# Performance work log

Measured on AMD Instinct MI355X. Metric: run time of the kernel, lower is better.

## Reference

```python
import jax, jax.numpy as jnp
import numpy as np

D = 512
H = 8
DH = D // H
FF = 2048
E = 4
EPS = 1e-5


def _layernorm(x, g, b):
    mu = jnp.mean(x, axis=-1, keepdims=True)
    var = jnp.mean(jnp.square(x - mu), axis=-1, keepdims=True)
    return (x - mu) * jax.lax.rsqrt(var + EPS) * g + b


def setup_inputs() -> dict:
    key = jax.random.key(0)
    ks = jax.random.split(key, 12)
    B, T = 4, 2048
    s = 0.02
    return {
        "x": jax.random.normal(ks[0], (B, T, D), jnp.float32),
        "fourier_bias": jax.random.normal(ks[1], (B, T, T), jnp.float32) * 0.1,
        "Wk": jax.random.normal(ks[2], (D, D), jnp.float32) * s,
        "bk": jnp.zeros((D,), jnp.float32),
        "Wv": jax.random.normal(ks[3], (D, D), jnp.float32) * s,
        "bv": jnp.zeros((D,), jnp.float32),
        "Wo": jax.random.normal(ks[4], (D, D), jnp.float32) * s,
        "bo": jnp.zeros((D,), jnp.float32),
        "ln1_g": jnp.ones((D,), jnp.float32),
        "ln1_b": jnp.zeros((D,), jnp.float32),
        "Wg": jax.random.normal(ks[5], (D, E), jnp.float32) * s,
        "bg": jnp.zeros((E,), jnp.float32),
        "W1": jax.random.normal(ks[6], (E, D, FF), jnp.float32) * s,
        "b1": jnp.zeros((E, FF), jnp.float32),
        "W2": jax.random.normal(ks[7], (E, FF, D), jnp.float32) * s,
        "b2": jnp.zeros((E, D), jnp.float32),
        "ln2_g": jnp.ones((D,), jnp.float32),
        "ln2_b": jnp.zeros((D,), jnp.float32),
    }


def reference(x, fourier_bias, Wk, bk, Wv, bv, Wo, bo, ln1_g, ln1_b,
              Wg, bg, W1, b1, W2, b2, ln2_g, ln2_b):
    B, T, _ = x.shape
    # --- Fourier pairwise-bias "attention" ---
    K = (x @ Wk + bk).reshape(B, T, H, DH).transpose(0, 2, 1, 3)  # [B,H,T,Dh]
    V = (x @ Wv + bv).reshape(B, T, H, DH).transpose(0, 2, 1, 3)  # [B,H,T,Dh]
    # sum_j (K_j + fb_ij) * V_j = sum_j K_j*V_j  +  sum_j fb_ij * V_j
    kv_sum = jnp.sum(K * V, axis=2, keepdims=True)                # [B,H,1,Dh]
    fbV = jnp.einsum('bij,bhjd->bhid', fourier_bias, V)           # [B,H,T,Dh]
    wv = (kv_sum + fbV).transpose(0, 2, 1, 3).reshape(B, T, D)
    x = _layernorm(x + (wv @ Wo + bo), ln1_g, ln1_b)
    # --- MoE FFN, top-2 gating (dropout/noise inactive in eval) ---
    scores = jax.nn.softmax(x @ Wg + bg, axis=-1)                 # [B,T,E]
    vals, idx = jax.lax.top_k(scores, 2)                          # [B,T,2]
    w = (jax.nn.one_hot(idx[..., 0], E, dtype=x.dtype) * vals[..., 0:1]
         + jax.nn.one_hot(idx[..., 1], E, dtype=x.dtype) * vals[..., 1:2])  # [B,T,E]
    h = jax.nn.relu(jnp.einsum('btd,edf->btef', x, W1) + b1)      # [B,T,E,FF]
    y = jnp.einsum('btef,efd->bted', h, W2) + b2                  # [B,T,E,D]
    ff = jnp.einsum('bte,bted->btd', w, y)
    return _layernorm(x + ff, ln2_g, ln2_b)
```

## Files before the change

kernel.cpp:

```cpp
#include <hip/hip_runtime.h>
#include <stdint.h>

#define BB   4
#define TT   2048
#define DD   512
#define FFF  2048
#define NEXP 4
#define NTOK (BB*TT)
#define LNEPS 1e-5f

typedef unsigned short u16;
typedef __attribute__((ext_vector_type(8))) short bf16x8;
typedef __attribute__((ext_vector_type(4))) float f32x4;

__device__ __forceinline__ u16 f2bf(float f) {
  union { float f; unsigned u; } v; v.f = f;
  return (u16)((v.u + 0x7FFFu + ((v.u >> 16) & 1u)) >> 16);
}
__device__ __forceinline__ float bf2f(u16 h) {
  union { unsigned u; float f; } v; v.u = (unsigned)h << 16; return v.f;
}

__device__ __forceinline__ void gl2lds(const u16* g, u16* l) {
  __builtin_amdgcn_global_load_lds(
      (const __attribute__((address_space(1))) void*)g,
      (__attribute__((address_space(3))) void*)l, 16, 0, 0);
}


__global__ void split_f32_kernel(const float* __restrict__ in, u16* __restrict__ hi,
                                 u16* __restrict__ lo, int n4) {
  int i = blockIdx.x * blockDim.x + threadIdx.x;
  if (i >= n4) return;
  float4 f = ((const float4*)in)[i];
  u16 h0 = f2bf(f.x), h1 = f2bf(f.y), h2 = f2bf(f.z), h3 = f2bf(f.w);
  u16 l0 = f2bf(f.x - bf2f(h0)), l1 = f2bf(f.y - bf2f(h1));
  u16 l2 = f2bf(f.z - bf2f(h2)), l3 = f2bf(f.w - bf2f(h3));
  ((uint2*)hi)[i] = uint2{(unsigned)h0 | ((unsigned)h1 << 16), (unsigned)h2 | ((unsigned)h3 << 16)};
  ((uint2*)lo)[i] = uint2{(unsigned)l0 | ((unsigned)l1 << 16), (unsigned)l2 | ((unsigned)l3 << 16)};
}

__global__ void transpose_split3_kernel(const float* __restrict__ s0, const float* __restrict__ s1,
                                        const float* __restrict__ s2,
                                        u16* __restrict__ kvhi, u16* __restrict__ kvlo,
                                        u16* __restrict__ ohi,  u16* __restrict__ olo) {
  __shared__ float tile[32][33];
  const int z = blockIdx.z;
  const float* in = (z == 0) ? s0 : (z == 1) ? s1 : s2;
  int c0 = blockIdx.x * 32, r0 = blockIdx.y * 32;
  int tx = threadIdx.x, ty = threadIdx.y;
#pragma unroll
  for (int k = 0; k < 4; k++)
    tile[ty + 8*k][tx] = in[(size_t)(r0 + ty + 8*k) * DD + c0 + tx];
  __syncthreads();
#pragma unroll
  for (int k = 0; k < 4; k++) {
    float v = tile[tx][ty + 8*k];
    u16 h = f2bf(v);
    u16 l = f2bf(v - bf2f(h));
    const int c = c0 + ty + 8*k;
    if (z < 2) {
      size_t idx = (size_t)(2*c + z) * DD + r0 + tx;
      kvhi[idx] = h; kvlo[idx] = l;
    } else {
      size_t idx = (size_t)c * DD + r0 + tx;
      ohi[idx] = h; olo[idx] = l;
    }
  }
}

__global__ void transpose_cast_kernel(const float* __restrict__ in, u16* __restrict__ out,
                                      int R, int C) {
  __shared__ float tile[32][33];
  int z = blockIdx.z;
  in  += (size_t)z * R * C;
  out += (size_t)z * R * C;
  int c0 = blockIdx.x * 32, r0 = blockIdx.y * 32;
  int tx = threadIdx.x, ty = threadIdx.y;
#pragma unroll
  for (int k = 0; k < 4; k++)
    tile[ty + 8*k][tx] = in[(size_t)(r0 + ty + 8*k) * C + c0 + tx];
  __syncthreads();
#pragma unroll
  for (int k = 0; k < 4; k++)
    out[(size_t)(c0 + ty + 8*k) * R + r0 + tx] = f2bf(tile[tx][ty + 8*k]);
}

template<int MODE>
__global__ __launch_bounds__(256)
void gemm_split2_kernel(const u16* __restrict__ Ahi, const u16* __restrict__ Alo,
                        const u16* __restrict__ Bhi, const u16* __restrict__ Blo,
                        const float* __restrict__ bias0, const float* __restrict__ bias1,
                        float* __restrict__ out0,
                        u16* __restrict__ outh, u16* __restrict__ outl,
                        int M, int N, int K,
                        long long sA, long long sB, long long sO) {
  constexpr int NBUF = (MODE == 2) ? 2 : 1;
  __shared__ u16 AhL[NBUF][128*32], AlL[NBUF][128*32];
  __shared__ u16 BhL[NBUF][64*32],  BlL[NBUF][64*32];

  int mt, nt, z;
  if constexpr (MODE == 2) {
    const int gid = blockIdx.x;
    const int xcd = gid & 7, slot = gid >> 3;
    z  = xcd >> 1;
    mt = (xcd & 1) + 2 * (slot >> 3);
    nt = slot & 7;
  } else {
    mt = blockIdx.x; nt = blockIdx.y; z = blockIdx.z;
  }
  const int m0 = mt * 128, n0 = nt * 64;

  Ahi += (size_t)z * sA; Alo += (size_t)z * sA;
  Bhi += (size_t)z * sB; Blo += (size_t)z * sB;
  const int tid = threadIdx.x;
  const int lane = tid & 63, wave = tid >> 6;
  const int wm = wave >> 1, wn = wave & 1;
  const int quad = lane >> 4, l16 = lane & 15;
  const int sxor = ((l16 >> 1) & 3) << 3;

  const int ar1 = tid >> 2;
  const int ac1 = (((tid & 3) ^ ((tid >> 3) & 3)) << 3);
  const u16* pAh1 = Ahi + (size_t)(m0 + ar1) * K + ac1;
  const u16* pAh2 = Ahi + (size_t)(m0 + ar1 + 64) * K + ac1;
  const u16* pAl1 = Alo + (size_t)(m0 + ar1) * K + ac1;
  const u16* pAl2 = Alo + (size_t)(m0 + ar1 + 64) * K + ac1;
  const u16* pBh1 = Bhi + (size_t)(n0 + ar1) * K + ac1;
  const u16* pBl1 = Blo + (size_t)(n0 + ar1) * K + ac1;
  const int wofs = wave * 512;

  f32x4 acc[4][2];
#pragma unroll
  for (int i = 0; i < 4; i++)
#pragma unroll
    for (int j = 0; j < 2; j++)
      acc[i][j] = f32x4{0.f, 0.f, 0.f, 0.f};

  const int NIT = K >> 5;
  if constexpr (MODE == 2) {
    gl2lds(pAh1, &AhL[0][wofs]); gl2lds(pAh2, &AhL[0][2048 + wofs]);
    gl2lds(pAl1, &AlL[0][wofs]); gl2lds(pAl2, &AlL[0][2048 + wofs]);
    gl2lds(pBh1, &BhL[0][wofs]); gl2lds(pBl1, &BlL[0][wofs]);
    for (int it = 0; it < NIT; it++) {
      const int buf = it & 1;
      __syncthreads();
      if (it + 1 < NIT) {
        const int ko = (it + 1) << 5;
        gl2lds(pAh1 + ko, &AhL[buf ^ 1][wofs]); gl2lds(pAh2 + ko, &AhL[buf ^ 1][2048 + wofs]);
        gl2lds(pAl1 + ko, &AlL[buf ^ 1][wofs]); gl2lds(pAl2 + ko, &AlL[buf ^ 1][2048 + wofs]);
        gl2lds(pBh1 + ko, &BhL[buf ^ 1][wofs]); gl2lds(pBl1 + ko, &BlL[buf ^ 1][wofs]);
      }
      bf16x8 afh[4], afl[4], bqh[2], bql[2];
#pragma unroll
      for (int i = 0; i < 4; i++) {
        afh[i] = *(const bf16x8*)&AhL[buf][(wm*64 + i*16 + l16) * 32 + (quad*8 ^ sxor)];
        afl[i] = *(const bf16x8*)&AlL[buf][(wm*64 + i*16 + l16) * 32 + (quad*8 ^ sxor)];
      }
#pragma unroll
      for (int j = 0; j < 2; j++) {
        bqh[j] = *(const bf16x8*)&BhL[buf][(wn*32 + j*16 + l16) * 32 + (quad*8 ^ sxor)];
        bql[j] = *(const bf16x8*)&BlL[buf][(wn*32 + j*16 + l16) * 32 + (quad*8 ^ sxor)];
      }
#pragma unroll
      for (int i = 0; i < 4; i++)
#pragma unroll
        for (int j = 0; j < 2; j++) {
          acc[i][j] = __builtin_amdgcn_mfma_f32_16x16x32_bf16(afh[i], bqh[j], acc[i][j], 0, 0, 0);
          acc[i][j] = __builtin_amdgcn_mfma_f32_16x16x32_bf16(afh[i], bql[j], acc[i][j], 0, 0, 0);
          acc[i][j] = __builtin_amdgcn_mfma_f32_16x16x32_bf16(afl[i], bqh[j], acc[i][j], 0, 0, 0);
        }
    }
  } else {
    for (int it = 0; it < NIT; it++) {
      const int ko = it << 5;
      __syncthreads();
      gl2lds(pAh1 + ko, &AhL[0][wofs]); gl2lds(pAh2 + ko, &AhL[0][2048 + wofs]);
      gl2lds(pAl1 + ko, &AlL[0][wofs]); gl2lds(pAl2 + ko, &AlL[0][2048 + wofs]);
      gl2lds(pBh1 + ko, &BhL[0][wofs]); gl2lds(pBl1 + ko, &BlL[0][wofs]);
      __syncthreads();
      bf16x8 afh[4], afl[4], bqh[2], bql[2];
#pragma unroll
      for (int i = 0; i < 4; i++) {
        afh[i] = *(const bf16x8*)&AhL[0][(wm*64 + i*16 + l16) * 32 + (quad*8 ^ sxor)];
        afl[i] = *(const bf16x8*)&AlL[0][(wm*64 + i*16 + l16) * 32 + (quad*8 ^ sxor)];
      }
#pragma unroll
      for (int j = 0; j < 2; j++) {
        bqh[j] = *(const bf16x8*)&BhL[0][(wn*32 + j*16 + l16) * 32 + (quad*8 ^ sxor)];
        bql[j] = *(const bf16x8*)&BlL[0][(wn*32 + j*16 + l16) * 32 + (quad*8 ^ sxor)];
      }
#pragma unroll
      for (int i = 0; i < 4; i++)
#pragma unroll
        for (int j = 0; j < 2; j++) {
          acc[i][j] = __builtin_amdgcn_mfma_f32_16x16x32_bf16(afh[i], bqh[j], acc[i][j], 0, 0, 0);
          acc[i][j] = __builtin_amdgcn_mfma_f32_16x16x32_bf16(afh[i], bql[j], acc[i][j], 0, 0, 0);
          acc[i][j] = __builtin_amdgcn_mfma_f32_16x16x32_bf16(afl[i], bqh[j], acc[i][j], 0, 0, 0);
        }
    }
  }

  if constexpr (MODE == 1) {
    const int b = m0 >> 11;
    const int rb0 = m0 & (TT - 1);
    const int colbase = n0 + wn*32 + l16;
    float kvp[2] = {0.f, 0.f};
#pragma unroll
    for (int i = 0; i < 4; i++) {
#pragma unroll
      for (int j = 0; j < 2; j++) {
        const int col = colbase + j*16;
        const int d = col >> 1;
        float vals[4];
#pragma unroll
        for (int r = 0; r < 4; r++) {
          float vv = acc[i][j][r] + ((col & 1) ? bias1[d] : bias0[d]);
          float pa = __shfl_xor(vv, 1);
          if (!(col & 1)) kvp[j] += vv * pa;
          vals[r] = vv;
        }
        if (col & 1) {
          const int rr = rb0 + wm*64 + i*16 + quad*4;
          u16 hs[4], ls[4];
#pragma unroll
          for (int r = 0; r < 4; r++) {
            hs[r] = f2bf(vals[r]);
            ls[r] = f2bf(vals[r] - bf2f(hs[r]));
          }
          size_t o = (size_t)b * DD * TT + (size_t)d * TT + rr;
          *(uint2*)&outh[o] = uint2{(unsigned)hs[0] | ((unsigned)hs[1]<<16),
                                    (unsigned)hs[2] | ((unsigned)hs[3]<<16)};
          *(uint2*)&outl[o] = uint2{(unsigned)ls[0] | ((unsigned)ls[1]<<16),
                                    (unsigned)ls[2] | ((unsigned)ls[3]<<16)};
        }
      }
    }
#pragma unroll
    for (int j = 0; j < 2; j++) {
      float p = kvp[j];
      p += __shfl_xor(p, 16);
      p += __shfl_xor(p, 32);
      const int col = colbase + j*16;
      if (!(col & 1) && quad == 0)
        atomicAdd(&out0[b * DD + (col >> 1)], p);
    }
  } else {
#pragma unroll
    for (int i = 0; i < 4; i++) {
#pragma unroll
      for (int r = 0; r < 4; r++) {
        const int row = m0 + wm*64 + i*16 + quad*4 + r;
#pragma unroll
        for (int j = 0; j < 2; j++) {
          const int col = n0 + wn*32 + j*16 + l16;
          float v = acc[i][j][r];
          if constexpr (MODE == 0) {
            out0[(size_t)row * N + col] = v + bias0[col];
          } else {
            v += bias0[(size_t)z * DD + col];
            u16 hv = f2bf(v);
            size_t idx = (size_t)z * sO + (size_t)row * DD + col;
            outh[idx] = hv;
            outl[idx] = f2bf(v - bf2f(hv));
          }
        }
      }
    }
  }
}

__global__ __launch_bounds__(256)
void moe_gemm1_kernel(const u16* __restrict__ X, const int* __restrict__ tokl,
                      const int* __restrict__ cnt, const u16* __restrict__ W1t,
                      const float* __restrict__ b1, u16* __restrict__ H) {
  const int e = blockIdx.z;
  int base = 0, cnte = 0;
#pragma unroll
  for (int i = 0; i < NEXP; i++) { int c = cnt[i]; if (i < e) base += c; if (i == e) cnte = c; }
  const int m0 = blockIdx.x * 128;
  if (m0 >= cnte) return;
  __shared__ u16 As[2][128*32], Bs[2][128*32];
  const int n0 = blockIdx.y * 128;
  const int tid = threadIdx.x, lane = tid & 63, wave = tid >> 6;
  const int wm = wave >> 1, wn = wave & 1, quad = lane >> 4, l16 = lane & 15;
  const int sxor = ((l16 >> 1) & 3) << 3;
  const int ar1 = tid >> 2;
  const int ac1 = (((tid & 3) ^ ((tid >> 3) & 3)) << 3);
  const int i1 = m0 + ar1 < cnte ? m0 + ar1 : cnte - 1;
  const int i2 = m0 + ar1 + 64 < cnte ? m0 + ar1 + 64 : cnte - 1;
  const int t1 = tokl[e * NTOK + i1], t2 = tokl[e * NTOK + i2];
  const u16* Bt = W1t + (size_t)e * DD * FFF;
  const float* bias = b1 + (size_t)e * FFF;
  const u16* pA1 = X + (size_t)t1 * DD + ac1;
  const u16* pA2 = X + (size_t)t2 * DD + ac1;
  const u16* pB1 = Bt + (size_t)(n0 + ar1) * DD + ac1;
  const u16* pB2 = Bt + (size_t)(n0 + ar1 + 64) * DD + ac1;
  const int wofs = wave * 512;

  f32x4 acc[4][4];
#pragma unroll
  for (int i = 0; i < 4; i++)
#pragma unroll
    for (int j = 0; j < 4; j++)
      acc[i][j] = f32x4{0.f, 0.f, 0.f, 0.f};

  const int NIT = DD >> 5;
  gl2lds(pA1, &As[0][wofs]); gl2lds(pA2, &As[0][2048 + wofs]);
  gl2lds(pB1, &Bs[0][wofs]); gl2lds(pB2, &Bs[0][2048 + wofs]);
  for (int it = 0; it < NIT; it++) {
    const int buf = it & 1;
    __syncthreads();
    if (it + 1 < NIT) {
      const int ko = (it + 1) << 5;
      gl2lds(pA1 + ko, &As[buf ^ 1][wofs]); gl2lds(pA2 + ko, &As[buf ^ 1][2048 + wofs]);
      gl2lds(pB1 + ko, &Bs[buf ^ 1][wofs]); gl2lds(pB2 + ko, &Bs[buf ^ 1][2048 + wofs]);
    }
    bf16x8 af[4], bq[4];
#pragma unroll
    for (int i = 0; i < 4; i++)
      af[i] = *(const bf16x8*)&As[buf][(wm*64 + i*16 + l16)*32 + (quad*8 ^ sxor)];
#pragma unroll
    for (int j = 0; j < 4; j++)
      bq[j] = *(const bf16x8*)&Bs[buf][(wn*64 + j*16 + l16)*32 + (quad*8 ^ sxor)];
#pragma unroll
    for (int i = 0; i < 4; i++)
#pragma unroll
      for (int j = 0; j < 4; j++)
        acc[i][j] = __builtin_amdgcn_mfma_f32_16x16x32_bf16(af[i], bq[j], acc[i][j], 0, 0, 0);
  }

#pragma unroll
  for (int i = 0; i < 4; i++) {
#pragma unroll
    for (int r = 0; r < 4; r++) {
      const int m = m0 + wm*64 + i*16 + quad*4 + r;
      if (m < cnte) {
#pragma unroll
        for (int j = 0; j < 4; j++) {
          const int col = n0 + wn*64 + j*16 + l16;
          H[(size_t)(base + m) * FFF + col] = f2bf(fmaxf(acc[i][j][r] + bias[col], 0.f));
        }
      }
    }
  }
}

__global__ __launch_bounds__(256)
void moe_gemm2_kernel(const u16* __restrict__ H, const int* __restrict__ tokl,
                      const int* __restrict__ cnt, const u16* __restrict__ W2t,
                      const float* __restrict__ b2, const float* __restrict__ wgt,
                      u16* __restrict__ Y) {
  const int e = blockIdx.z;
  int base = 0, cnte = 0;
#pragma unroll
  for (int i = 0; i < NEXP; i++) { int c = cnt[i]; if (i < e) base += c; if (i == e) cnte = c; }
  const int m0 = blockIdx.x * 128;
  if (m0 >= cnte) return;
  __shared__ u16 As[2][128*32], Bs[2][128*32];
  const int n0 = blockIdx.y * 128;
  const int tid = threadIdx.x, lane = tid & 63, wave = tid >> 6;
  const int wm = wave >> 1, wn = wave & 1, quad = lane >> 4, l16 = lane & 15;
  const int sxor = ((l16 >> 1) & 3) << 3;
  const int ar1 = tid >> 2;
  const int ac1 = (((tid & 3) ^ ((tid >> 3) & 3)) << 3);
  const int i1 = m0 + ar1 < cnte ? m0 + ar1 : cnte - 1;
  const int i2 = m0 + ar1 + 64 < cnte ? m0 + ar1 + 64 : cnte - 1;
  const u16* Bt = W2t + (size_t)e * FFF * DD;
  const float* bias = b2 + (size_t)e * DD;
  const u16* pA1 = H + (size_t)(base + i1) * FFF + ac1;
  const u16* pA2 = H + (size_t)(base + i2) * FFF + ac1;
  const u16* pB1 = Bt + (size_t)(n0 + ar1) * FFF + ac1;
  const u16* pB2 = Bt + (size_t)(n0 + ar1 + 64) * FFF + ac1;
  const int wofs = wave * 512;

  f32x4 acc[4][4];
#pragma unroll
  for (int i = 0; i < 4; i++)
#pragma unroll
    for (int j = 0; j < 4; j++)
      acc[i][j] = f32x4{0.f, 0.f, 0.f, 0.f};

  const int NIT = FFF >> 5;
  gl2lds(pA1, &As[0][wofs]); gl2lds(pA2, &As[0][2048 + wofs]);
  gl2lds(pB1, &Bs[0][wofs]); gl2lds(pB2, &Bs[0][2048 + wofs]);
  for (int it = 0; it < NIT; it++) {
    const int buf = it & 1;
    __syncthreads();
    if (it + 1 < NIT) {
      const int ko = (it + 1) << 5;
      gl2lds(pA1 + ko, &As[buf ^ 1][wofs]); gl2lds(pA2 + ko, &As[buf ^ 1][2048 + wofs]);
      gl2lds(pB1 + ko, &Bs[buf ^ 1][wofs]); gl2lds(pB2 + ko, &Bs[buf ^ 1][2048 + wofs]);
    }
    bf16x8 af[4], bq[4];
#pragma unroll
    for (int i = 0; i < 4; i++)
      af[i] = *(const bf16x8*)&As[buf][(wm*64 + i*16 + l16)*32 + (quad*8 ^ sxor)];
#pragma unroll
    for (int j = 0; j < 4; j++)
      bq[j] = *(const bf16x8*)&Bs[buf][(wn*64 + j*16 + l16)*32 + (quad*8 ^ sxor)];
#pragma unroll
    for (int i = 0; i < 4; i++)
#pragma unroll
      for (int j = 0; j < 4; j++)
        acc[i][j] = __builtin_amdgcn_mfma_f32_16x16x32_bf16(af[i], bq[j], acc[i][j], 0, 0, 0);
  }

#pragma unroll
  for (int i = 0; i < 4; i++) {
#pragma unroll
    for (int r = 0; r < 4; r++) {
      const int m = m0 + wm*64 + i*16 + quad*4 + r;
      if (m < cnte) {
        const int t = tokl[e * NTOK + m];
        const float w = wgt[(size_t)t * NEXP + e];
#pragma unroll
        for (int j = 0; j < 4; j++) {
          const int col = n0 + wn*64 + j*16 + l16;
          Y[(size_t)(base + m) * DD + col] = f2bf((acc[i][j][r] + bias[col]) * w);
        }
      }
    }
  }
}

__global__ void ln_kernel(const float* __restrict__ a, const float* __restrict__ b,
                          const float* __restrict__ g, const float* __restrict__ beta,
                          float* __restrict__ outf, u16* __restrict__ outb) {
  int t = blockIdx.x;
  int tid = threadIdx.x;
  float v0 = a[(size_t)t*DD + tid]       + b[(size_t)t*DD + tid];
  float v1 = a[(size_t)t*DD + 256 + tid] + b[(size_t)t*DD + 256 + tid];
  float s = v0 + v1, s2 = v0*v0 + v1*v1;
  for (int off = 32; off; off >>= 1) { s += __shfl_down(s, off); s2 += __shfl_down(s2, off); }
  __shared__ float ws[4], ws2[4];
  if ((tid & 63) == 0) { ws[tid >> 6] = s; ws2[tid >> 6] = s2; }
  __syncthreads();
  if (tid == 0) {
    float ts = 0, ts2 = 0;
    for (int i = 0; i < 4; i++) { ts += ws[i]; ts2 += ws2[i]; }
    ws[0] = ts; ws2[0] = ts2;
  }
  __syncthreads();
  float mean = ws[0] * (1.f / DD);
  float var  = ws2[0] * (1.f / DD) - mean * mean;
  float rstd = rsqrtf(var + LNEPS);
  float o0 = (v0 - mean) * rstd * g[tid]       + beta[tid];
  float o1 = (v1 - mean) * rstd * g[256 + tid] + beta[256 + tid];
  outf[(size_t)t*DD + tid]       = o0;
  outf[(size_t)t*DD + 256 + tid] = o1;
  outb[(size_t)t*DD + tid]       = f2bf(o0);
  outb[(size_t)t*DD + 256 + tid] = f2bf(o1);
}

__global__ void ln2_kernel(const float* __restrict__ x1, const u16* __restrict__ Y,
                           const int* __restrict__ tokslot, const int* __restrict__ cnt,
                           const float* __restrict__ g, const float* __restrict__ beta,
                           float* __restrict__ out) {
  int t = blockIdx.x;
  int tid = threadIdx.x;
  const int c0 = cnt[0], c1 = cnt[1], c2 = cnt[2];
  const int s0 = tokslot[2*t], s1 = tokslot[2*t + 1];
  const int e0 = s0 >> 14, k0 = s0 & 16383;
  const int e1 = s1 >> 14, k1 = s1 & 16383;
  const int b0 = (e0 > 0 ? c0 : 0) + (e0 > 1 ? c1 : 0) + (e0 > 2 ? c2 : 0);
  const int b1 = (e1 > 0 ? c0 : 0) + (e1 > 1 ? c1 : 0) + (e1 > 2 ? c2 : 0);
  const u16* y0 = Y + (size_t)(b0 + k0) * DD;
  const u16* y1 = Y + (size_t)(b1 + k1) * DD;
  float v0 = x1[(size_t)t*DD + tid]       + bf2f(y0[tid])       + bf2f(y1[tid]);
  float v1 = x1[(size_t)t*DD + 256 + tid] + bf2f(y0[256 + tid]) + bf2f(y1[256 + tid]);
  float s = v0 + v1, s2 = v0*v0 + v1*v1;
  for (int off = 32; off; off >>= 1) { s += __shfl_down(s, off); s2 += __shfl_down(s2, off); }
  __shared__ float ws[4], ws2[4];
  if ((tid & 63) == 0) { ws[tid >> 6] = s; ws2[tid >> 6] = s2; }
  __syncthreads();
  if (tid == 0) {
    float ts = 0, ts2 = 0;
    for (int i = 0; i < 4; i++) { ts += ws[i]; ts2 += ws2[i]; }
    ws[0] = ts; ws2[0] = ts2;
  }
  __syncthreads();
  float mean = ws[0] * (1.f / DD);
  float var  = ws2[0] * (1.f / DD) - mean * mean;
  float rstd = rsqrtf(var + LNEPS);
  out[(size_t)t*DD + tid]       = (v0 - mean) * rstd * g[tid]       + beta[tid];
  out[(size_t)t*DD + 256 + tid] = (v1 - mean) * rstd * g[256 + tid] + beta[256 + tid];
}

__global__ __launch_bounds__(256)
void gate_kernel(const float* __restrict__ x1, const float* __restrict__ Wg,
                 const float* __restrict__ bg, float* __restrict__ wfull,
                 int* __restrict__ tokl, int* __restrict__ cnt, int* __restrict__ tokslot) {
  __shared__ int lcnt[NEXP];
  __shared__ int lbase[NEXP];
  __shared__ int lslots[NEXP][128];
  const int tid = threadIdx.x, lane = tid & 63, wave = tid >> 6;
  if (tid < NEXP) lcnt[tid] = 0;
  __syncthreads();
  const int tblk = blockIdx.x * 64;
  for (int i = 0; i < 16; i++) {
    const int t = tblk + wave * 16 + i;
    float s0 = 0.f, s1 = 0.f, s2 = 0.f, s3 = 0.f;
    for (int d = lane; d < DD; d += 64) {
      float xv = x1[(size_t)t * DD + d];
      float4 w = *(const float4*)&Wg[d * 4];
      s0 += xv * w.x; s1 += xv * w.y; s2 += xv * w.z; s3 += xv * w.w;
    }
    for (int off = 32; off; off >>= 1) {
      s0 += __shfl_down(s0, off); s1 += __shfl_down(s1, off);
      s2 += __shfl_down(s2, off); s3 += __shfl_down(s3, off);
    }
    if (lane == 0) {
      float sc[4] = {s0 + bg[0], s1 + bg[1], s2 + bg[2], s3 + bg[3]};
      float mx = fmaxf(fmaxf(sc[0], sc[1]), fmaxf(sc[2], sc[3]));
      float sum = 0.f;
      for (int e = 0; e < 4; e++) { sc[e] = expf(sc[e] - mx); sum += sc[e]; }
      float inv = 1.f / sum;
      for (int e = 0; e < 4; e++) sc[e] *= inv;
      int i0 = 0;
      for (int e = 1; e < 4; e++) if (sc[e] > sc[i0]) i0 = e;
      int i1 = -1;
      for (int e = 0; e < 4; e++) { if (e == i0) continue; if (i1 < 0 || sc[e] > sc[i1]) i1 = e; }
      float w[4] = {0.f, 0.f, 0.f, 0.f};
      w[i0] = sc[i0]; w[i1] = sc[i1];
      *(float4*)&wfull[(size_t)t * 4] = float4{w[0], w[1], w[2], w[3]};
      int p0 = atomicAdd(&lcnt[i0], 1); lslots[i0][p0] = (t << 1);
      int p1 = atomicAdd(&lcnt[i1], 1); lslots[i1][p1] = (t << 1) | 1;
    }
  }
  __syncthreads();
  if (tid < NEXP) lbase[tid] = atomicAdd(&cnt[tid], lcnt[tid]);
  __syncthreads();
  for (int idx = tid; idx < NEXP * 128; idx += 256) {
    const int e = idx >> 7, p = idx & 127;
    if (p < lcnt[e]) {
      const int v = lslots[e][p];
      const int t = v >> 1;
      const int pos = lbase[e] + p;
      tokl[e * NTOK + pos] = t;
      tokslot[2 * t + (v & 1)] = (e << 14) | pos;
    }
  }
}

extern "C" void kernel_launch(void* const* d_in, const int* in_sizes, int n_in,
                              void* d_out, int out_size, void* d_ws, size_t ws_size,
                              hipStream_t stream) {
  const float* x    = (const float*)d_in[0];
  const float* fb   = (const float*)d_in[1];
  const float* Wk   = (const float*)d_in[2];
  const float* bk   = (const float*)d_in[3];
  const float* Wv   = (const float*)d_in[4];
  const float* bv   = (const float*)d_in[5];
  const float* Wo   = (const float*)d_in[6];
  const float* bo   = (const float*)d_in[7];
  const float* ln1g = (const float*)d_in[8];
  const float* ln1b = (const float*)d_in[9];
  const float* Wg   = (const float*)d_in[10];
  const float* bg   = (const float*)d_in[11];
  const float* W1   = (const float*)d_in[12];
  const float* b1   = (const float*)d_in[13];
  const float* W2   = (const float*)d_in[14];
  const float* b2   = (const float*)d_in[15];
  const float* ln2g = (const float*)d_in[16];
  const float* ln2b = (const float*)d_in[17];

  const size_t MiB = 1048576;
  char* ws = (char*)d_ws;
  char* R1 = ws;
  u16* xhi  = (u16*)R1;             u16* xlo  = (u16*)(R1 + 8*MiB);
  u16* wvhi = (u16*)R1;             u16* wvlo = (u16*)(R1 + 8*MiB);
  u16* x1b  = (u16*)R1;
  char* R2 = ws + 16*MiB;
  u16* fbhi = (u16*)R2;             u16* fblo = (u16*)(R2 + 32*MiB);
  u16* h    = (u16*)R2;
  char* R3 = ws + 80*MiB;
  u16* vthi   = (u16*)R3;           u16* vtlo  = (u16*)(R3 + 8*MiB);
  float* attn = (float*)R3;
  u16*  yb    = (u16*)R3;
  float* x1f  = (float*)(R3 + 16*MiB);
  char* R4 = ws + 112*MiB;
  u16* wkvthi = (u16*)R4;
  u16* wkvtlo = (u16*)(R4 + 1*MiB);
  u16* wothi  = (u16*)(R4 + 2*MiB);
  u16* wotlo  = (u16*)(R4 + 2*MiB + 512*1024);
  u16* w1t    = (u16*)(R4 + 3*MiB);
  u16* w2t    = (u16*)(R4 + 11*MiB);
  char* R5 = ws + 131*MiB;
  float* kvs    = (float*)R5;
  int*   cnt    = (int*)(R5 + 8192);
  float* wfull  = (float*)(R5 + 16*1024);
  int*   tokl   = (int*)(R5 + 160*1024);
  int*   tokslot= (int*)(R5 + 320*1024);
  (void)ws_size; (void)in_sizes; (void)n_in; (void)out_size;

  dim3 tb(32, 8);

  hipMemsetAsync(kvs, 0, 8192 + 16, stream);

  split_f32_kernel<<<NTOK * DD / 4 / 256, 256, 0, stream>>>(x, xhi, xlo, NTOK * DD / 4);
  split_f32_kernel<<<BB * TT * TT / 4 / 256, 256, 0, stream>>>(fb, fbhi, fblo, BB * TT * TT / 4);
  transpose_split3_kernel<<<dim3(16, 16, 3), tb, 0, stream>>>(Wk, Wv, Wo,
                                                              wkvthi, wkvtlo, wothi, wotlo);
  transpose_cast_kernel<<<dim3(FFF/32, DD/32, NEXP), tb, 0, stream>>>(W1, w1t, DD, FFF);
  transpose_cast_kernel<<<dim3(DD/32, FFF/32, NEXP), tb, 0, stream>>>(W2, w2t, FFF, DD);

  gemm_split2_kernel<1><<<dim3(64, 16, 1), 256, 0, stream>>>(
      xhi, xlo, wkvthi, wkvtlo, bk, bv, kvs, vthi, vtlo,
      NTOK, 2*DD, DD, 0, 0, 0);

  gemm_split2_kernel<2><<<dim3(512, 1, 1), 256, 0, stream>>>(
      fbhi, fblo, vthi, vtlo, kvs, nullptr, nullptr, wvhi, wvlo,
      TT, DD, TT, (long long)TT*TT, (long long)DD*TT, (long long)TT*DD);

  gemm_split2_kernel<0><<<dim3(64, 8, 1), 256, 0, stream>>>(
      wvhi, wvlo, wothi, wotlo, bo, nullptr, attn, nullptr, nullptr,
      NTOK, DD, DD, 0, 0, 0);

  ln_kernel<<<NTOK, 256, 0, stream>>>(x, attn, ln1g, ln1b, x1f, x1b);

  gate_kernel<<<NTOK / 64, 256, 0, stream>>>(x1f, Wg, bg, wfull, tokl, cnt, tokslot);

  moe_gemm1_kernel<<<dim3(NTOK/128, FFF/128, NEXP), 256, 0, stream>>>(
      x1b, tokl, cnt, w1t, b1, h);
  moe_gemm2_kernel<<<dim3(NTOK/128, DD/128, NEXP), 256, 0, stream>>>(
      h, tokl, cnt, w2t, b2, wfull, yb);

  ln2_kernel<<<NTOK, 256, 0, stream>>>(x1f, yb, tokslot, cnt, ln2g, ln2b, (float*)d_out);
}
```

Measured before the change: 510.7 us.

## Fuse fourier_bias hi/lo split into the fbV GEMM operand load

Removes the separate pass that split the 64 MiB fp32 fourier_bias into bf16 hi/lo arrays. A dedicated fbV kernel now loads fp32 tiles directly into LDS and splits them into hi/lo bf16 fragments in registers, using packed convert instructions. This drops one full read and 32 MiB of writes plus a later 32 MiB re-read of the split arrays. In exchange the A tile in LDS is twice as large, each K step does extra ALU conversion work, and the generic GEMM loses its MODE 2 path.

```diff
diff --git a/kernel.cpp b/kernel.cpp
--- a/kernel.cpp
+++ b/kernel.cpp
@@ -25,6 +25,40 @@
   __builtin_amdgcn_global_load_lds(
       (const __attribute__((address_space(1))) void*)g,
       (__attribute__((address_space(3))) void*)l, 16, 0, 0);
+}
+__device__ __forceinline__ void gl2lds_f(const float* g, float* l) {
+  __builtin_amdgcn_global_load_lds(
+      (const __attribute__((address_space(1))) void*)g,
+      (__attribute__((address_space(3))) void*)l, 16, 0, 0);
+}
+
+__device__ __forceinline__ unsigned cvtpk_bf16(float a, float b) {
+  unsigned r;
+  asm volatile("v_cvt_pk_bf16_f32 %0, %1, %2" : "=v"(r) : "v"(a), "v"(b));
+  return r;
+}
+__device__ __forceinline__ void split2x4(f32x4 a0, f32x4 a1, bf16x8* hi, bf16x8* lo) {
+  union U { unsigned u[4]; bf16x8 v; };
+  U H, L;
+  H.u[0] = cvtpk_bf16(a0[0], a0[1]);
+  H.u[1] = cvtpk_bf16(a0[2], a0[3]);
+  H.u[2] = cvtpk_bf16(a1[0], a1[1]);
+  H.u[3] = cvtpk_bf16(a1[2], a1[3]);
+  union F { unsigned u; float f; } t0, t1;
+  float l0,l1,l2,l3,l4,l5,l6,l7;
+  t0.u = H.u[0] << 16;         l0 = a0[0] - t0.f;
+  t1.u = H.u[0] & 0xffff0000u; l1 = a0[1] - t1.f;
+  t0.u = H.u[1] << 16;         l2 = a0[2] - t0.f;
+  t1.u = H.u[1] & 0xffff0000u; l3 = a0[3] - t1.f;
+  t0.u = H.u[2] << 16;         l4 = a1[0] - t0.f;
+  t1.u = H.u[2] & 0xffff0000u; l5 = a1[1] - t1.f;
+  t0.u = H.u[3] << 16;         l6 = a1[2] - t0.f;
+  t1.u = H.u[3] & 0xffff0000u; l7 = a1[3] - t1.f;
+  L.u[0] = cvtpk_bf16(l0, l1);
+  L.u[1] = cvtpk_bf16(l2, l3);
+  L.u[2] = cvtpk_bf16(l4, l5);
+  L.u[3] = cvtpk_bf16(l6, l7);
+  *hi = H.v; *lo = L.v;
 }
 
 
@@ -95,20 +129,10 @@
                         u16* __restrict__ outh, u16* __restrict__ outl,
                         int M, int N, int K,
                         long long sA, long long sB, long long sO) {
-  constexpr int NBUF = (MODE == 2) ? 2 : 1;
-  __shared__ u16 AhL[NBUF][128*32], AlL[NBUF][128*32];
-  __shared__ u16 BhL[NBUF][64*32],  BlL[NBUF][64*32];
-
-  int mt, nt, z;
-  if constexpr (MODE == 2) {
-    const int gid = blockIdx.x;
-    const int xcd = gid & 7, slot = gid >> 3;
-    z  = xcd >> 1;
-    mt = (xcd & 1) + 2 * (slot >> 3);
-    nt = slot & 7;
-  } else {
-    mt = blockIdx.x; nt = blockIdx.y; z = blockIdx.z;
-  }
+  __shared__ u16 AhL[128*32], AlL[128*32];
+  __shared__ u16 BhL[64*32],  BlL[64*32];
+
+  const int mt = blockIdx.x, nt = blockIdx.y, z = blockIdx.z;
   const int m0 = mt * 128, n0 = nt * 64;
 
   Ahi += (size_t)z * sA; Alo += (size_t)z * sA;
@@ -137,67 +161,32 @@
       acc[i][j] = f32x4{0.f, 0.f, 0.f, 0.f};
 
   const int NIT = K >> 5;
-  if constexpr (MODE == 2) {
-    gl2lds(pAh1, &AhL[0][wofs]); gl2lds(pAh2, &AhL[0][2048 + wofs]);
-    gl2lds(pAl1, &AlL[0][wofs]); gl2lds(pAl2, &AlL[0][2048 + wofs]);
-    gl2lds(pBh1, &BhL[0][wofs]); gl2lds(pBl1, &BlL[0][wofs]);
-    for (int it = 0; it < NIT; it++) {
-      const int buf = it & 1;
-      __syncthreads();
-      if (it + 1 < NIT) {
-        const int ko = (it + 1) << 5;
-        gl2lds(pAh1 + ko, &AhL[buf ^ 1][wofs]); gl2lds(pAh2 + ko, &AhL[buf ^ 1][2048 + wofs]);
-        gl2lds(pAl1 + ko, &AlL[buf ^ 1][wofs]); gl2lds(pAl2 + ko, &AlL[buf ^ 1][2048 + wofs]);
-        gl2lds(pBh1 + ko, &BhL[buf ^ 1][wofs]); gl2lds(pBl1 + ko, &BlL[buf ^ 1][wofs]);
+  for (int it = 0; it < NIT; it++) {
+    const int ko = it << 5;
+    __syncthreads();
+    gl2lds(pAh1 + ko, &AhL[wofs]); gl2lds(pAh2 + ko, &AhL[2048 + wofs]);
+    gl2lds(pAl1 + ko, &AlL[wofs]); gl2lds(pAl2 + ko, &AlL[2048 + wofs]);
+    gl2lds(pBh1 + ko, &BhL[wofs]); gl2lds(pBl1 + ko, &BlL[wofs]);
+    __syncthreads();
+    bf16x8 afh[4], afl[4], bqh[2], bql[2];
+#pragma unroll
+    for (int i = 0; i < 4; i++) {
+      afh[i] = *(const bf16x8*)&AhL[(wm*64 + i*16 + l16) * 32 + (quad*8 ^ sxor)];
+      afl[i] = *(const bf16x8*)&AlL[(wm*64 + i*16 + l16) * 32 + (quad*8 ^ sxor)];
+    }
+#pragma unroll
+    for (int j = 0; j < 2; j++) {
+      bqh[j] = *(const bf16x8*)&BhL[(wn*32 + j*16 + l16) * 32 + (quad*8 ^ sxor)];
+      bql[j] = *(const bf16x8*)&BlL[(wn*32 + j*16 + l16) * 32 + (quad*8 ^ sxor)];
+    }
+#pragma unroll
+    for (int i = 0; i < 4; i++)
+#pragma unroll
+      for (int j = 0; j < 2; j++) {
+        acc[i][j] = __builtin_amdgcn_mfma_f32_16x16x32_bf16(afh[i], bqh[j], acc[i][j], 0, 0, 0);
+        acc[i][j] = __builtin_amdgcn_mfma_f32_16x16x32_bf16(afh[i], bql[j], acc[i][j], 0, 0, 0);
+        acc[i][j] = __builtin_amdgcn_mfma_f32_16x16x32_bf16(afl[i], bqh[j], acc[i][j], 0, 0, 0);
       }
-      bf16x8 afh[4], afl[4], bqh[2], bql[2];
-#pragma unroll
-      for (int i = 0; i < 4; i++) {
-        afh[i] = *(const bf16x8*)&AhL[buf][(wm*64 + i*16 + l16) * 32 + (quad*8 ^ sxor)];
-        afl[i] = *(const bf16x8*)&AlL[buf][(wm*64 + i*16 + l16) * 32 + (quad*8 ^ sxor)];
-      }
-#pragma unroll
-      for (int j = 0; j < 2; j++) {
-        bqh[j] = *(const bf16x8*)&BhL[buf][(wn*32 + j*16 + l16) * 32 + (quad*8 ^ sxor)];
-        bql[j] = *(const bf16x8*)&BlL[buf][(wn*32 + j*16 + l16) * 32 + (quad*8 ^ sxor)];
-      }
-#pragma unroll
-      for (int i = 0; i < 4; i++)
-#pragma unroll
-        for (int j = 0; j < 2; j++) {
-          acc[i][j] = __builtin_amdgcn_mfma_f32_16x16x32_bf16(afh[i], bqh[j], acc[i][j], 0, 0, 0);
-          acc[i][j] = __builtin_amdgcn_mfma_f32_16x16x32_bf16(afh[i], bql[j], acc[i][j], 0, 0, 0);
-          acc[i][j] = __builtin_amdgcn_mfma_f32_16x16x32_bf16(afl[i], bqh[j], acc[i][j], 0, 0, 0);
-        }
-    }
-  } else {
-    for (int it = 0; it < NIT; it++) {
-      const int ko = it << 5;
-      __syncthreads();
-      gl2lds(pAh1 + ko, &AhL[0][wofs]); gl2lds(pAh2 + ko, &AhL[0][2048 + wofs]);
-      gl2lds(pAl1 + ko, &AlL[0][wofs]); gl2lds(pAl2 + ko, &AlL[0][2048 + wofs]);
-      gl2lds(pBh1 + ko, &BhL[0][wofs]); gl2lds(pBl1 + ko, &BlL[0][wofs]);
-      __syncthreads();
-      bf16x8 afh[4], afl[4], bqh[2], bql[2];
-#pragma unroll
-      for (int i = 0; i < 4; i++) {
-        afh[i] = *(const bf16x8*)&AhL[0][(wm*64 + i*16 + l16) * 32 + (quad*8 ^ sxor)];
-        afl[i] = *(const bf16x8*)&AlL[0][(wm*64 + i*16 + l16) * 32 + (quad*8 ^ sxor)];
-      }
-#pragma unroll
-      for (int j = 0; j < 2; j++) {
-        bqh[j] = *(const bf16x8*)&BhL[0][(wn*32 + j*16 + l16) * 32 + (quad*8 ^ sxor)];
-        bql[j] = *(const bf16x8*)&BlL[0][(wn*32 + j*16 + l16) * 32 + (quad*8 ^ sxor)];
-      }
-#pragma unroll
-      for (int i = 0; i < 4; i++)
-#pragma unroll
-        for (int j = 0; j < 2; j++) {
-          acc[i][j] = __builtin_amdgcn_mfma_f32_16x16x32_bf16(afh[i], bqh[j], acc[i][j], 0, 0, 0);
-          acc[i][j] = __builtin_amdgcn_mfma_f32_16x16x32_bf16(afh[i], bql[j], acc[i][j], 0, 0, 0);
-          acc[i][j] = __builtin_amdgcn_mfma_f32_16x16x32_bf16(afl[i], bqh[j], acc[i][j], 0, 0, 0);
-        }
-    }
   }
 
   if constexpr (MODE == 1) {
@@ -253,17 +242,102 @@
 #pragma unroll
         for (int j = 0; j < 2; j++) {
           const int col = n0 + wn*32 + j*16 + l16;
-          float v = acc[i][j][r];
-          if constexpr (MODE == 0) {
-            out0[(size_t)row * N + col] = v + bias0[col];
-          } else {
-            v += bias0[(size_t)z * DD + col];
-            u16 hv = f2bf(v);
-            size_t idx = (size_t)z * sO + (size_t)row * DD + col;
-            outh[idx] = hv;
-            outl[idx] = f2bf(v - bf2f(hv));
-          }
+          out0[(size_t)row * N + col] = acc[i][j][r] + bias0[col];
         }
+      }
+    }
+  }
+}
+
+__global__ __launch_bounds__(256)
+void fbv_kernel(const float* __restrict__ FB,
+                const u16* __restrict__ Bhi, const u16* __restrict__ Blo,
+                const float* __restrict__ kvs,
+                u16* __restrict__ outh, u16* __restrict__ outl) {
+  __shared__ float Af[2][128*32];
+  __shared__ u16 BhL[2][64*32], BlL[2][64*32];
+  const int gid = blockIdx.x;
+  const int xcd = gid & 7, slot = gid >> 3;
+  const int z  = xcd >> 1;
+  const int mt = (xcd & 1) + 2 * (slot >> 3);
+  const int nt = slot & 7;
+  const int m0 = mt * 128, n0 = nt * 64;
+  const float* A = FB + (size_t)z * TT * TT;
+  const u16* Bh = Bhi + (size_t)z * DD * TT;
+  const u16* Bl = Blo + (size_t)z * DD * TT;
+  const int tid = threadIdx.x, lane = tid & 63, wave = tid >> 6;
+  const int wm = wave >> 1, wn = wave & 1, quad = lane >> 4, l16 = lane & 15;
+  const int sxor = ((l16 >> 1) & 3) << 3;
+  const int x7 = l16 & 7;
+
+  const int arf = tid >> 3;
+  const int acf = (((tid & 7) ^ (arf & 7)) << 2);
+  const float* pA = A + (size_t)(m0 + arf) * TT + acf;
+  const int ar1 = tid >> 2;
+  const int ac1 = (((tid & 3) ^ ((tid >> 3) & 3)) << 3);
+  const u16* pBh = Bh + (size_t)(n0 + ar1) * TT + ac1;
+  const u16* pBl = Bl + (size_t)(n0 + ar1) * TT + ac1;
+  const int wofs = wave * 512;
+  const int wofsA = wave << 8;
+
+  f32x4 acc[4][2];
+#pragma unroll
+  for (int i = 0; i < 4; i++)
+#pragma unroll
+    for (int j = 0; j < 2; j++)
+      acc[i][j] = f32x4{0.f, 0.f, 0.f, 0.f};
+
+  const int NIT = TT >> 5;
+#pragma unroll
+  for (int c = 0; c < 4; c++)
+    gl2lds_f(pA + (size_t)c * 32 * TT, &Af[0][c*1024 + wofsA]);
+  gl2lds(pBh, &BhL[0][wofs]); gl2lds(pBl, &BlL[0][wofs]);
+  for (int it = 0; it < NIT; it++) {
+    const int buf = it & 1;
+    __syncthreads();
+    if (it + 1 < NIT) {
+      const int ko = (it + 1) << 5;
+#pragma unroll
+      for (int c = 0; c < 4; c++)
+        gl2lds_f(pA + (size_t)c * 32 * TT + ko, &Af[buf ^ 1][c*1024 + wofsA]);
+      gl2lds(pBh + ko, &BhL[buf ^ 1][wofs]); gl2lds(pBl + ko, &BlL[buf ^ 1][wofs]);
+    }
+    bf16x8 afh[4], afl[4], bqh[2], bql[2];
+#pragma unroll
+    for (int i = 0; i < 4; i++) {
+      const int rowR = wm*64 + i*16 + l16;
+      f32x4 a0 = *(const f32x4*)&Af[buf][rowR*32 + ((((quad << 1)    ) ^ x7) << 2)];
+      f32x4 a1 = *(const f32x4*)&Af[buf][rowR*32 + ((((quad << 1) | 1) ^ x7) << 2)];
+      split2x4(a0, a1, &afh[i], &afl[i]);
+    }
+#pragma unroll
+    for (int j = 0; j < 2; j++) {
+      bqh[j] = *(const bf16x8*)&BhL[buf][(wn*32 + j*16 + l16) * 32 + (quad*8 ^ sxor)];
+      bql[j] = *(const bf16x8*)&BlL[buf][(wn*32 + j*16 + l16) * 32 + (quad*8 ^ sxor)];
+    }
+#pragma unroll
+    for (int i = 0; i < 4; i++)
+#pragma unroll
+      for (int j = 0; j < 2; j++) {
+        acc[i][j] = __builtin_amdgcn_mfma_f32_16x16x32_bf16(afh[i], bqh[j], acc[i][j], 0, 0, 0);
+        acc[i][j] = __builtin_amdgcn_mfma_f32_16x16x32_bf16(afh[i], bql[j], acc[i][j], 0, 0, 0);
+        acc[i][j] = __builtin_amdgcn_mfma_f32_16x16x32_bf16(afl[i], bqh[j], acc[i][j], 0, 0, 0);
+      }
+  }
+
+#pragma unroll
+  for (int i = 0; i < 4; i++) {
+#pragma unroll
+    for (int r = 0; r < 4; r++) {
+      const int row = m0 + wm*64 + i*16 + quad*4 + r;
+#pragma unroll
+      for (int j = 0; j < 2; j++) {
+        const int col = n0 + wn*32 + j*16 + l16;
+        float v = acc[i][j][r] + kvs[z * DD + col];
+        u16 hv = f2bf(v);
+        size_t idx = (size_t)z * TT * DD + (size_t)row * DD + col;
+        outh[idx] = hv;
+        outl[idx] = f2bf(v - bf2f(hv));
       }
     }
   }
@@ -571,7 +645,6 @@
   u16* wvhi = (u16*)R1;             u16* wvlo = (u16*)(R1 + 8*MiB);
   u16* x1b  = (u16*)R1;
   char* R2 = ws + 16*MiB;
-  u16* fbhi = (u16*)R2;             u16* fblo = (u16*)(R2 + 32*MiB);
   u16* h    = (u16*)R2;
   char* R3 = ws + 80*MiB;
   u16* vthi   = (u16*)R3;           u16* vtlo  = (u16*)(R3 + 8*MiB);
@@ -598,7 +671,6 @@
   hipMemsetAsync(kvs, 0, 8192 + 16, stream);
 
   split_f32_kernel<<<NTOK * DD / 4 / 256, 256, 0, stream>>>(x, xhi, xlo, NTOK * DD / 4);
-  split_f32_kernel<<<BB * TT * TT / 4 / 256, 256, 0, stream>>>(fb, fbhi, fblo, BB * TT * TT / 4);
   transpose_split3_kernel<<<dim3(16, 16, 3), tb, 0, stream>>>(Wk, Wv, Wo,
                                                               wkvthi, wkvtlo, wothi, wotlo);
   transpose_cast_kernel<<<dim3(FFF/32, DD/32, NEXP), tb, 0, stream>>>(W1, w1t, DD, FFF);
@@ -608,9 +680,7 @@
       xhi, xlo, wkvthi, wkvtlo, bk, bv, kvs, vthi, vtlo,
       NTOK, 2*DD, DD, 0, 0, 0);
 
-  gemm_split2_kernel<2><<<dim3(512, 1, 1), 256, 0, stream>>>(
-      fbhi, fblo, vthi, vtlo, kvs, nullptr, nullptr, wvhi, wvlo,
-      TT, DD, TT, (long long)TT*TT, (long long)DD*TT, (long long)TT*DD);
+  fbv_kernel<<<dim3(512, 1, 1), 256, 0, stream>>>(fb, vthi, vtlo, kvs, wvhi, wvlo);
 
   gemm_split2_kernel<0><<<dim3(64, 8, 1), 256, 0, stream>>>(
       wvhi, wvlo, wothi, wotlo, bo, nullptr, attn, nullptr, nullptr,
```

New measurement: 527.1 us. 1.03x slower.
